# Kernel tuning notes

Hardware: AMD Instinct MI355X
Metric: run time of the kernel (lower is better)

The kernel has to match this reference:

```python
import jax, jax.numpy as jnp
import numpy as np

B, N, IN_CH = 16, 2048, 128
H, C = 4, 64
HC = H * C
E = 524288
NT = B * N
FC0, FC1 = 1024, 512
OMIC = 128
OUT = 2
LN_EPS = 1e-5


def setup_inputs() -> dict:
    key = jax.random.key(0)
    ks = jax.random.split(key, 32)
    s = 0.02
    d = {}
    d['x'] = jax.random.normal(ks[0], (NT, IN_CH), jnp.float32)
    d['edge_index'] = jax.random.randint(ks[1], (2, E), 0, NT, dtype=jnp.int64)
    # GATConv 1: Linear(IN_CH, H*C, bias=False), att_src/att_dst [H,C], bias [H*C]
    d['w1'] = jax.random.normal(ks[2], (IN_CH, HC), jnp.float32) * s
    d['att_src1'] = jax.random.normal(ks[3], (H, C), jnp.float32) * s
    d['att_dst1'] = jax.random.normal(ks[4], (H, C), jnp.float32) * s
    d['bias1'] = jnp.zeros((HC,), jnp.float32)
    d['pool1_w'] = jax.random.normal(ks[5], (HC, 1), jnp.float32) * s
    d['pool1_b'] = jnp.zeros((1,), jnp.float32)
    # GATConv 2: in = H*C
    d['w2'] = jax.random.normal(ks[6], (HC, HC), jnp.float32) * s
    d['att_src2'] = jax.random.normal(ks[7], (H, C), jnp.float32) * s
    d['att_dst2'] = jax.random.normal(ks[8], (H, C), jnp.float32) * s
    d['bias2'] = jnp.zeros((HC,), jnp.float32)
    d['pool2_w'] = jax.random.normal(ks[9], (HC, 1), jnp.float32) * s
    d['pool2_b'] = jnp.zeros((1,), jnp.float32)
    # LayerNorm(num_nodes)
    d['ln_w'] = jnp.ones((N,), jnp.float32)
    d['ln_b'] = jnp.zeros((N,), jnp.float32)
    # FC encoder: Linear(3N, FC0)+ELU, Linear(FC0, FC1)+ELU, Linear(FC1, OMIC)+ELU
    d['enc0_w'] = jax.random.normal(ks[10], (3 * N, FC0), jnp.float32) * s
    d['enc0_b'] = jnp.zeros((FC0,), jnp.float32)
    d['enc1_w'] = jax.random.normal(ks[11], (FC0, FC1), jnp.float32) * s
    d['enc1_b'] = jnp.zeros((FC1,), jnp.float32)
    d['enc2_w'] = jax.random.normal(ks[12], (FC1, OMIC), jnp.float32) * s
    d['enc2_b'] = jnp.zeros((OMIC,), jnp.float32)
    d['last_w'] = jax.random.normal(ks[13], (OMIC, OUT), jnp.float32) * s
    d['last_b'] = jnp.zeros((OUT,), jnp.float32)
    return d


def layer_norm(v, w, b):
    mu = jnp.mean(v, axis=-1, keepdims=True)
    var = jnp.mean((v - mu) ** 2, axis=-1, keepdims=True)
    return (v - mu) * jax.lax.rsqrt(var + LN_EPS) * w + b


def gat_conv(x, src, dst, w, att_src, att_dst, bias):
    # x: [NT, F_in] -> transformed per head [NT, H, C]
    xw = (x @ w).reshape(NT, H, C)
    a_src = jnp.einsum('nhc,hc->nh', xw, att_src)  # [NT, H]
    a_dst = jnp.einsum('nhc,hc->nh', xw, att_dst)
    alpha = jax.nn.leaky_relu(a_src[src] + a_dst[dst], negative_slope=0.2)  # [E', H]
    amax = jax.ops.segment_max(alpha, dst, num_segments=NT)
    ea = jnp.exp(alpha - amax[dst])
    denom = jax.ops.segment_sum(ea, dst, num_segments=NT)
    coef = ea / (denom[dst] + 1e-16)
    msg = xw[src] * coef[:, :, None]  # [E', H, C]
    out = jax.ops.segment_sum(msg, dst, num_segments=NT)
    return out.reshape(NT, HC) + bias


def reference(x, edge_index, w1, att_src1, att_dst1, bias1, pool1_w, pool1_b,
              w2, att_src2, att_dst2, bias2, pool2_w, pool2_b,
              ln_w, ln_b, enc0_w, enc0_b, enc1_w, enc1_b, enc2_w, enc2_b,
              last_w, last_b):
    # add self-loops (GATConv default)
    loops = jnp.arange(NT, dtype=edge_index.dtype)
    src = jnp.concatenate([edge_index[0], loops])
    dst = jnp.concatenate([edge_index[1], loops])
    # layer1 feature: per-node mean, densified to [B, N]
    x0 = layer_norm(jnp.mean(x, axis=-1).reshape(B, N), ln_w, ln_b)
    # GAT layer 1 (dropout is identity in eval)
    h = jax.nn.elu(gat_conv(x, src, dst, w1, att_src1, att_dst1, bias1))
    x1 = layer_norm((h @ pool1_w + pool1_b)[:, 0].reshape(B, N), ln_w, ln_b)
    # GAT layer 2
    h = jax.nn.elu(gat_conv(h, src, dst, w2, att_src2, att_dst2, bias2))
    x2 = layer_norm((h @ pool2_w + pool2_b)[:, 0].reshape(B, N), ln_w, ln_b)
    feat = jnp.concatenate([x0, x1, x2], axis=1)  # [B, 3N]
    e = jax.nn.elu(feat @ enc0_w + enc0_b)
    e = jax.nn.elu(e @ enc1_w + enc1_b)
    e = jax.nn.elu(e @ enc2_w + enc2_b)
    return e @ last_w + last_b  # [B, OUT]
```

## Files before the change

kernel.cpp:

```cpp
#include <hip/hip_runtime.h>
#include <math.h>

#define NTN 32768
#define BB 16
#define NN 2048
#define IN_CH 128
#define HC 256
#define EREAL 524288
#define ETOT (EREAL + NTN)
#define FC0 1024
#define FC1 512
#define OMIC 128
#define OUTD 2
#define CAP 96

#define PREP_BLKS (NTN / 4)
#define DEG_BLKS (EREAL / 256)
#define CASTW_BLKS ((HC * IN_CH + HC * HC) / 256)
#define GEMM_YB (NTN / 128)
#define FILL_YB 512

typedef __attribute__((ext_vector_type(8))) short bf16x8;
typedef __attribute__((ext_vector_type(4))) float f32x4;
typedef __attribute__((ext_vector_type(2))) float f32x2;

static __device__ __forceinline__ float wave_sum(float v) {
    for (int o = 32; o; o >>= 1) v += __shfl_xor(v, o);
    return v;
}
static __device__ __forceinline__ unsigned short f2bf(float f) {
    unsigned u = __float_as_uint(f);
    unsigned r = (u + 0x7fff + ((u >> 16) & 1)) >> 16;
    return (unsigned short)r;
}
static __device__ __forceinline__ void wave_sync() {
    asm volatile("s_waitcnt lgkmcnt(0)" ::: "memory");
    __builtin_amdgcn_sched_barrier(0);
}
static __device__ __forceinline__ void pkfma(f32x2& acc, f32x2 ab, f32x2 e2) {
    asm("v_pk_fma_f32 %0, %1, %2, %0" : "+v"(acc) : "v"(ab), "v"(e2));
}
static __device__ __forceinline__ void fma8pk(uint4 v, f32x2 e2, f32x2* acc) {
    f32x2 p;
    p.x = __uint_as_float(v.x << 16); p.y = __uint_as_float(v.x & 0xffff0000u);
    pkfma(acc[0], p, e2);
    p.x = __uint_as_float(v.y << 16); p.y = __uint_as_float(v.y & 0xffff0000u);
    pkfma(acc[1], p, e2);
    p.x = __uint_as_float(v.z << 16); p.y = __uint_as_float(v.z & 0xffff0000u);
    pkfma(acc[2], p, e2);
    p.x = __uint_as_float(v.w << 16); p.y = __uint_as_float(v.w & 0xffff0000u);
    pkfma(acc[3], p, e2);
}
static __device__ __forceinline__ void dot2bf(float& acc, unsigned px, unsigned pe) {
    asm("v_dot2_f32_bf16 %0, %1, %2, %0" : "+v"(acc) : "v"(px), "v"(pe));
}
static __device__ __forceinline__ void dot8x2(uint4 a, uint4 b, unsigned pe, float* acc) {
    unsigned p;
    p = __builtin_amdgcn_perm(a.x, b.x, 0x01000504u); dot2bf(acc[0], p, pe);
    p = __builtin_amdgcn_perm(a.x, b.x, 0x03020706u); dot2bf(acc[1], p, pe);
    p = __builtin_amdgcn_perm(a.y, b.y, 0x01000504u); dot2bf(acc[2], p, pe);
    p = __builtin_amdgcn_perm(a.y, b.y, 0x03020706u); dot2bf(acc[3], p, pe);
    p = __builtin_amdgcn_perm(a.z, b.z, 0x01000504u); dot2bf(acc[4], p, pe);
    p = __builtin_amdgcn_perm(a.z, b.z, 0x03020706u); dot2bf(acc[5], p, pe);
    p = __builtin_amdgcn_perm(a.w, b.w, 0x01000504u); dot2bf(acc[6], p, pe);
    p = __builtin_amdgcn_perm(a.w, b.w, 0x03020706u); dot2bf(acc[7], p, pe);
}

__global__ __launch_bounds__(256) void k_pre(
    const float* __restrict__ x, unsigned short* __restrict__ xb, float* __restrict__ xmean,
    const int* __restrict__ ei, int* __restrict__ deg, int* __restrict__ epos,
    const float* __restrict__ w1, const float* __restrict__ w2,
    unsigned short* __restrict__ w1t, unsigned short* __restrict__ w2t) {
    int b = blockIdx.x, t = threadIdx.x;
    if (b < PREP_BLKS) {
        int wave = t >> 6, lane = t & 63;
        int n = b * 4 + wave;
        float2 v = *(const float2*)(x + (size_t)n * IN_CH + lane * 2);
        ushort2 o;
        o.x = f2bf(v.x); o.y = f2bf(v.y);
        *(ushort2*)(xb + (size_t)n * IN_CH + lane * 2) = o;
        float s = wave_sum(v.x + v.y);
        if (lane == 0) xmean[n] = s * (1.0f / 128.0f);
    } else if (b < PREP_BLKS + DEG_BLKS) {
        int e = (b - PREP_BLKS) * 256 + t;
        int d = ei[EREAL + e];
        epos[e] = atomicAdd(&deg[d], 1);
    } else {
        int idx = (b - PREP_BLKS - DEG_BLKS) * 256 + t;
        if (idx < HC * IN_CH) {
            int n = idx / IN_CH, k = idx % IN_CH;
            w1t[idx] = f2bf(w1[(size_t)k * HC + n]);
        } else {
            int j = idx - HC * IN_CH;
            int n = j / HC, k = j % HC;
            w2t[j] = f2bf(w2[(size_t)k * HC + n]);
        }
    }
}

__global__ __launch_bounds__(1024) void k_scan(const int* __restrict__ deg, int* __restrict__ rowptr,
                                               int* __restrict__ csr) {
    __shared__ int sd[1024];
    int t = threadIdx.x;
    int base = t * 32;
    int loc[32];
    int s = 0;
#pragma unroll
    for (int j = 0; j < 32; j++) { int d = deg[base + j] + 1; loc[j] = d; s += d; }
    sd[t] = s; __syncthreads();
    for (int o = 1; o < 1024; o <<= 1) {
        int v = (t >= o) ? sd[t - o] : 0;
        __syncthreads();
        sd[t] += v;
        __syncthreads();
    }
    int run = sd[t] - s;
#pragma unroll
    for (int j = 0; j < 32; j++) {
        rowptr[base + j] = run;
        csr[run] = base + j;
        run += loc[j];
    }
    if (t == 1023) rowptr[NTN] = run;
}

__global__ __launch_bounds__(256) void k_gemm_mfma(
    const unsigned short* __restrict__ A, const unsigned short* __restrict__ Bt, int K,
    const float* __restrict__ attS, const float* __restrict__ attD,
    unsigned short* __restrict__ Cout, float* __restrict__ aS, float* __restrict__ aD,
    const int* __restrict__ ei, const int* __restrict__ epos,
    const int* __restrict__ rowptr, int* __restrict__ csr) {
    __shared__ unsigned short As[128][72];
    __shared__ unsigned short Bs[64][72];
    const int t = threadIdx.x;
    const int bx = blockIdx.x, by = blockIdx.y;
    if (by >= GEMM_YB) {
        int e = (((by - GEMM_YB) * 4 + bx)) * 256 + t;
        int s = ei[e], d = ei[EREAL + e];
        csr[rowptr[d] + 1 + epos[e]] = s;
        return;
    }
    const int lane = t & 63, wave = t >> 6;
    const int quad = lane >> 4, l16 = lane & 15;
    const int arow = t >> 1, acol = (t & 1) * 32;
    const int brow = t >> 2, bcol = (t & 3) * 16;
    const unsigned short* Ag = A + (size_t)(by * 128 + arow) * K + acol;
    const unsigned short* Bg = Bt + (size_t)(bx * 64 + brow) * K + bcol;
    f32x4 acc[2][4] = {};
    for (int k0 = 0; k0 < K; k0 += 64) {
        uint4 a0 = *(const uint4*)(Ag + k0);
        uint4 a1 = *(const uint4*)(Ag + k0 + 8);
        uint4 a2 = *(const uint4*)(Ag + k0 + 16);
        uint4 a3 = *(const uint4*)(Ag + k0 + 24);
        uint4 b0 = *(const uint4*)(Bg + k0);
        uint4 b1 = *(const uint4*)(Bg + k0 + 8);
        __syncthreads();
        *(uint4*)&As[arow][acol +  0] = a0;
        *(uint4*)&As[arow][acol +  8] = a1;
        *(uint4*)&As[arow][acol + 16] = a2;
        *(uint4*)&As[arow][acol + 24] = a3;
        *(uint4*)&Bs[brow][bcol +  0] = b0;
        *(uint4*)&Bs[brow][bcol +  8] = b1;
        __syncthreads();
#pragma unroll
        for (int kc = 0; kc < 64; kc += 32) {
            bf16x8 af[2], bfr[4];
#pragma unroll
            for (int mt = 0; mt < 2; mt++)
                af[mt] = *(const bf16x8*)&As[wave * 32 + mt * 16 + l16][kc + quad * 8];
#pragma unroll
            for (int nt = 0; nt < 4; nt++)
                bfr[nt] = *(const bf16x8*)&Bs[nt * 16 + l16][kc + quad * 8];
#pragma unroll
            for (int mt = 0; mt < 2; mt++)
#pragma unroll
                for (int nt = 0; nt < 4; nt++)
                    acc[mt][nt] = __builtin_amdgcn_mfma_f32_16x16x32_bf16(af[mt], bfr[nt], acc[mt][nt], 0, 0, 0);
        }
    }
    float as_l[4], ad_l[4];
#pragma unroll
    for (int nt = 0; nt < 4; nt++) {
        int gcol = bx * 64 + nt * 16 + l16;
        as_l[nt] = attS[gcol];
        ad_l[nt] = attD[gcol];
    }
#pragma unroll
    for (int mt = 0; mt < 2; mt++) {
#pragma unroll
        for (int reg = 0; reg < 4; reg++) {
            int grow = by * 128 + wave * 32 + mt * 16 + quad * 4 + reg;
            float ps = 0.f, pd = 0.f;
#pragma unroll
            for (int nt = 0; nt < 4; nt++) {
                float v = acc[mt][nt][reg];
                Cout[(size_t)grow * HC + bx * 64 + nt * 16 + l16] = f2bf(v);
                ps += v * as_l[nt];
                pd += v * ad_l[nt];
            }
            for (int o = 8; o; o >>= 1) { ps += __shfl_xor(ps, o); pd += __shfl_xor(pd, o); }
            if (l16 == 0) { aS[grow * 4 + bx] = ps; aD[grow * 4 + bx] = pd; }
        }
    }
}

__global__ __launch_bounds__(256) void k_agg(
    const unsigned short* __restrict__ xw, const float* __restrict__ aS, const float* __restrict__ aD,
    const int* __restrict__ rowptr, const int* __restrict__ csr,
    const float* __restrict__ bias, const float* __restrict__ poolw, const float* __restrict__ poolb,
    unsigned short* __restrict__ hout, float* __restrict__ xpre) {
    __shared__ float ea_s[4][CAP][4];
    __shared__ int   ss[4][CAP];
    int t = threadIdx.x;
    int w = t >> 6, lane = t & 63;
    int n = blockIdx.x * 4 + w;
    int beg = rowptr[n], end = rowptr[n + 1];
    int deg = end - beg;
    float4 ad4 = *(const float4*)(aD + n * 4);
    float l0 = 0.f, l1 = 0.f, l2 = 0.f, l3 = 0.f;
    if (deg <= CAP) {
        for (int i = lane; i < deg; i += 64) {
            int s = csr[beg + i];
            ss[w][i] = s << 9;
            float4 as4 = *(const float4*)(aS + s * 4);
            float a0 = as4.x + ad4.x; a0 = a0 > 0.f ? a0 : 0.2f * a0;
            float a1 = as4.y + ad4.y; a1 = a1 > 0.f ? a1 : 0.2f * a1;
            float a2 = as4.z + ad4.z; a2 = a2 > 0.f ? a2 : 0.2f * a2;
            float a3 = as4.w + ad4.w; a3 = a3 > 0.f ? a3 : 0.2f * a3;
            float4 e4;
            e4.x = __expf(a0); e4.y = __expf(a1); e4.z = __expf(a2); e4.w = __expf(a3);
            *(float4*)&ea_s[w][i][0] = e4;
        }
        wave_sync();
    } else {
        for (int i = lane; i < deg; i += 64) {
            int s = csr[beg + i];
            float4 as4 = *(const float4*)(aS + s * 4);
            float a0 = as4.x + ad4.x; a0 = a0 > 0.f ? a0 : 0.2f * a0; l0 += __expf(a0);
            float a1 = as4.y + ad4.y; a1 = a1 > 0.f ? a1 : 0.2f * a1; l1 += __expf(a1);
            float a2 = as4.z + ad4.z; a2 = a2 > 0.f ? a2 : 0.2f * a2; l2 += __expf(a2);
            float a3 = as4.w + ad4.w; a3 = a3 > 0.f ? a3 : 0.2f * a3; l3 += __expf(a3);
        }
        l0 = wave_sum(l0); l1 = wave_sum(l1); l2 = wave_sum(l2); l3 = wave_sum(l3);
    }
    int l31 = lane & 31, hi = lane >> 5;
    int head = l31 >> 3;
    float acc8[8] = {};
    f32x2 accF[4] = {};
    unsigned tb = (unsigned)(l31 * 16);
    const char* xwb_ = (const char*)xw;
    if (deg <= CAP) {
        int i = 0;
        for (; i + 16 <= deg; i += 16) {
            int iA = i + 8 * hi;
            int o0 = ss[w][iA], o1 = ss[w][iA + 1], o2 = ss[w][iA + 2], o3 = ss[w][iA + 3];
            int o4 = ss[w][iA + 4], o5 = ss[w][iA + 5], o6 = ss[w][iA + 6], o7 = ss[w][iA + 7];
            float e0 = ea_s[w][iA][head],     e1 = ea_s[w][iA + 1][head];
            float e2 = ea_s[w][iA + 2][head], e3 = ea_s[w][iA + 3][head];
            float e4 = ea_s[w][iA + 4][head], e5 = ea_s[w][iA + 5][head];
            float e6 = ea_s[w][iA + 6][head], e7 = ea_s[w][iA + 7][head];
            uint4 v0 = *(const uint4*)(xwb_ + ((unsigned)o0 + tb));
            uint4 v1 = *(const uint4*)(xwb_ + ((unsigned)o1 + tb));
            uint4 v2 = *(const uint4*)(xwb_ + ((unsigned)o2 + tb));
            uint4 v3 = *(const uint4*)(xwb_ + ((unsigned)o3 + tb));
            uint4 v4 = *(const uint4*)(xwb_ + ((unsigned)o4 + tb));
            uint4 v5 = *(const uint4*)(xwb_ + ((unsigned)o5 + tb));
            uint4 v6 = *(const uint4*)(xwb_ + ((unsigned)o6 + tb));
            uint4 v7 = *(const uint4*)(xwb_ + ((unsigned)o7 + tb));
            unsigned p01, p23, p45, p67;
            asm("v_cvt_pk_bf16_f32 %0, %1, %2" : "=v"(p01) : "v"(e0), "v"(e1));
            asm("v_cvt_pk_bf16_f32 %0, %1, %2" : "=v"(p23) : "v"(e2), "v"(e3));
            asm("v_cvt_pk_bf16_f32 %0, %1, %2" : "=v"(p45) : "v"(e4), "v"(e5));
            asm("v_cvt_pk_bf16_f32 %0, %1, %2" : "=v"(p67) : "v"(e6), "v"(e7));
            dot8x2(v0, v1, p01, acc8);
            dot8x2(v2, v3, p23, acc8);
            dot8x2(v4, v5, p45, acc8);
            dot8x2(v6, v7, p67, acc8);
        }
        for (; i + 8 <= deg; i += 8) {
            int iA = i + 4 * hi;
            int o0 = ss[w][iA], o1 = ss[w][iA + 1], o2 = ss[w][iA + 2], o3 = ss[w][iA + 3];
            float e0 = ea_s[w][iA][head],     e1 = ea_s[w][iA + 1][head];
            float e2 = ea_s[w][iA + 2][head], e3 = ea_s[w][iA + 3][head];
            uint4 v0 = *(const uint4*)(xwb_ + ((unsigned)o0 + tb));
            uint4 v1 = *(const uint4*)(xwb_ + ((unsigned)o1 + tb));
            uint4 v2 = *(const uint4*)(xwb_ + ((unsigned)o2 + tb));
            uint4 v3 = *(const uint4*)(xwb_ + ((unsigned)o3 + tb));
            unsigned p01, p23;
            asm("v_cvt_pk_bf16_f32 %0, %1, %2" : "=v"(p01) : "v"(e0), "v"(e1));
            asm("v_cvt_pk_bf16_f32 %0, %1, %2" : "=v"(p23) : "v"(e2), "v"(e3));
            dot8x2(v0, v1, p01, acc8);
            dot8x2(v2, v3, p23, acc8);
        }
        for (; i + 4 <= deg; i += 4) {
            int iA = i + 2 * hi;
            int o0 = ss[w][iA], o1 = ss[w][iA + 1];
            float e0 = ea_s[w][iA][head], e1 = ea_s[w][iA + 1][head];
            unsigned pe;
            asm("v_cvt_pk_bf16_f32 %0, %1, %2" : "=v"(pe) : "v"(e0), "v"(e1));
            uint4 v0 = *(const uint4*)(xwb_ + ((unsigned)o0 + tb));
            uint4 v1 = *(const uint4*)(xwb_ + ((unsigned)o1 + tb));
            dot8x2(v0, v1, pe, acc8);
        }
        if (i < deg) {
            int iA = i + 2 * hi, iB = iA + 1;
            bool okA = iA < deg, okB = iB < deg;
            int ia = okA ? iA : 0;
            int ib = okB ? iB : 0;
            int o0 = ss[w][ia], o1 = ss[w][ib];
            float e0 = okA ? ea_s[w][ia][head] : 0.f;
            float e1 = okB ? ea_s[w][ib][head] : 0.f;
            unsigned pe;
            asm("v_cvt_pk_bf16_f32 %0, %1, %2" : "=v"(pe) : "v"(e0), "v"(e1));
            uint4 v0 = *(const uint4*)(xwb_ + ((unsigned)o0 + tb));
            uint4 v1 = *(const uint4*)(xwb_ + ((unsigned)o1 + tb));
            dot8x2(v0, v1, pe, acc8);
        }
    } else {
        const unsigned short* xwc = xw + l31 * 8;
        float adh = head == 0 ? ad4.x : head == 1 ? ad4.y : head == 2 ? ad4.z : ad4.w;
        for (int i = beg; i < end; i += 2) {
            int idx = i + hi;
            bool ok = idx < end;
            int sA = csr[ok ? idx : beg];
            float a = aS[sA * 4 + head] + adh;
            a = a > 0.f ? a : 0.2f * a;
            float eA = ok ? __expf(a) : 0.f;
            uint4 vA = *(const uint4*)(xwc + (size_t)sA * HC);
            f32x2 eA2; eA2.x = eA; eA2.y = eA;
            fma8pk(vA, eA2, accF);
        }
    }
    float r8[8];
#pragma unroll
    for (int j = 0; j < 8; j++) {
        float v = acc8[j] + accF[j >> 1][j & 1];
        v += __shfl_xor(v, 32);
        r8[j] = v;
    }
    if (hi == 0) {
        float ilh;
        if (deg <= CAP) {
            float lsum = 0.f;
            for (int j = (l31 & 7); j < deg; j += 8) lsum += ea_s[w][j][head];
            lsum += __shfl_xor(lsum, 1);
            lsum += __shfl_xor(lsum, 2);
            lsum += __shfl_xor(lsum, 4);
            ilh = 1.0f / (lsum + 1e-16f);
        } else {
            float lh = head == 0 ? l0 : head == 1 ? l1 : head == 2 ? l2 : l3;
            ilh = 1.0f / (lh + 1e-16f);
        }
        float4 b0 = *(const float4*)(bias + l31 * 8);
        float4 b1 = *(const float4*)(bias + l31 * 8 + 4);
        float r[8];
        r[0] = r8[0] * ilh + b0.x;
        r[1] = r8[1] * ilh + b0.y;
        r[2] = r8[2] * ilh + b0.z;
        r[3] = r8[3] * ilh + b0.w;
        r[4] = r8[4] * ilh + b1.x;
        r[5] = r8[5] * ilh + b1.y;
        r[6] = r8[6] * ilh + b1.z;
        r[7] = r8[7] * ilh + b1.w;
#pragma unroll
        for (int j = 0; j < 8; j++) r[j] = r[j] > 0.f ? r[j] : expm1f(r[j]);
        if (hout) {
            uint4 o;
            o.x = (unsigned)f2bf(r[0]) | ((unsigned)f2bf(r[1]) << 16);
            o.y = (unsigned)f2bf(r[2]) | ((unsigned)f2bf(r[3]) << 16);
            o.z = (unsigned)f2bf(r[4]) | ((unsigned)f2bf(r[5]) << 16);
            o.w = (unsigned)f2bf(r[6]) | ((unsigned)f2bf(r[7]) << 16);
            *(uint4*)(hout + (size_t)n * HC + l31 * 8) = o;
        }
        float4 w0 = *(const float4*)(poolw + l31 * 8);
        float4 w1v = *(const float4*)(poolw + l31 * 8 + 4);
        float p = r[0] * w0.x + r[1] * w0.y + r[2] * w0.z + r[3] * w0.w +
                  r[4] * w1v.x + r[5] * w1v.y + r[6] * w1v.z + r[7] * w1v.w;
        for (int o = 16; o; o >>= 1) p += __shfl_xor(p, o);
        if (l31 == 0) xpre[n] = p + poolb[0];
    }
}

__global__ __launch_bounds__(256) void k_ln3(const float* __restrict__ xmean, const float* __restrict__ x1pre,
                                             const float* __restrict__ x2pre, const float* __restrict__ lw,
                                             const float* __restrict__ lb, float* __restrict__ feat) {
    __shared__ float r0[256], r1[256];
    int b = blockIdx.x, t = threadIdx.x;
    int row = b & 15, seg = b >> 4;
    const float* src = (seg == 0 ? xmean : seg == 1 ? x1pre : x2pre) + (size_t)row * NN;
    float* dst = feat + (size_t)row * (3 * NN) + seg * NN;
    float v[8];
    float s = 0.f, s2 = 0.f;
#pragma unroll
    for (int j = 0; j < 8; j++) {
        float x = src[t + j * 256];
        v[j] = x; s += x; s2 += x * x;
    }
    r0[t] = s; r1[t] = s2; __syncthreads();
    for (int o = 128; o; o >>= 1) {
        if (t < o) { r0[t] += r0[t + o]; r1[t] += r1[t + o]; }
        __syncthreads();
    }
    float mu = r0[0] * (1.0f / NN);
    float var = r1[0] * (1.0f / NN) - mu * mu;
    float rs = rsqrtf(var + 1e-5f);
#pragma unroll
    for (int j = 0; j < 8; j++) {
        int idx = t + j * 256;
        dst[idx] = (v[j] - mu) * rs * lw[idx] + lb[idx];
    }
}

template<int KC>
__global__ __launch_bounds__(256) void k_fc_splitk(const float* __restrict__ In, const float* __restrict__ W,
                                                   float* __restrict__ partial, int K, int Nc) {
    __shared__ float in_s[16][KC];
    int t = threadIdx.x;
    int k0 = blockIdx.y * KC;
    for (int idx = t; idx < 16 * KC; idx += 256) {
        int r = idx / KC, kk = idx % KC;
        in_s[r][kk] = In[(size_t)r * K + k0 + kk];
    }
    __syncthreads();
    int col = blockIdx.x * 256 + t;
    if (col < Nc) {
        float acc[16] = {};
#pragma unroll
        for (int kk = 0; kk < KC; kk++) {
            float w = W[(size_t)(k0 + kk) * Nc + col];
#pragma unroll
            for (int r = 0; r < 16; r++) acc[r] += in_s[r][kk] * w;
        }
        float* pp = partial + ((size_t)blockIdx.y * 16) * Nc + col;
#pragma unroll
        for (int r = 0; r < 16; r++) pp[(size_t)r * Nc] = acc[r];
    }
}

__global__ __launch_bounds__(256) void k_fc1(
    const float* __restrict__ part0, const float* __restrict__ b0,
    const float* __restrict__ W, float* __restrict__ partial) {
    __shared__ float in_s[16][16];
    int t = threadIdx.x;
    int bx = blockIdx.x, by = blockIdx.y;
    int k0 = by * 16;
    {
        int r = t >> 4, kk = t & 15;
        float s = 0.f;
#pragma unroll 8
        for (int k = 0; k < 96; k++) s += part0[((size_t)(k * 16) + r) * FC0 + (k0 + kk)];
        s += b0[k0 + kk];
        in_s[r][kk] = s > 0.f ? s : expm1f(s);
    }
    __syncthreads();
    int col = bx * 256 + t;
    float acc[16] = {};
#pragma unroll
    for (int kk = 0; kk < 16; kk++) {
        float wv = W[(size_t)(k0 + kk) * FC1 + col];
#pragma unroll
        for (int r = 0; r < 16; r++) acc[r] += in_s[r][kk] * wv;
    }
    float* pp = partial + ((size_t)by * 16) * FC1 + col;
#pragma unroll
    for (int r = 0; r < 16; r++) pp[(size_t)r * FC1] = acc[r];
}

__global__ __launch_bounds__(256) void k_fc2(
    const float* __restrict__ part1, const float* __restrict__ b1,
    const float* __restrict__ W, float* __restrict__ partial) {
    __shared__ float in_s[16][16];
    int t = threadIdx.x;
    int by = blockIdx.x;
    int k0 = by * 16;
    {
        int r = t >> 4, kk = t & 15;
        float s = 0.f;
#pragma unroll 8
        for (int k = 0; k < 64; k++) s += part1[((size_t)(k * 16) + r) * FC1 + (k0 + kk)];
        s += b1[k0 + kk];
        in_s[r][kk] = s > 0.f ? s : expm1f(s);
    }
    __syncthreads();
    if (t < OMIC) {
        int col = t;
        float acc[16] = {};
#pragma unroll
        for (int kk = 0; kk < 16; kk++) {
            float wv = W[(size_t)(k0 + kk) * OMIC + col];
#pragma unroll
            for (int r = 0; r < 16; r++) acc[r] += in_s[r][kk] * wv;
        }
        float* pp = partial + ((size_t)by * 16) * OMIC + col;
#pragma unroll
        for (int r = 0; r < 16; r++) pp[(size_t)r * OMIC] = acc[r];
    }
}

__global__ __launch_bounds__(256) void k_last2(
    const float* __restrict__ part2, const float* __restrict__ b2,
    const float* __restrict__ W, const float* __restrict__ bl, float* __restrict__ Out) {
    __shared__ float e2s[16][OMIC];
    int t = threadIdx.x;
    for (int idx = t; idx < 16 * OMIC; idx += 256) {
        int r = idx >> 7, c = idx & 127;
        float s = 0.f;
#pragma unroll 8
        for (int k = 0; k < 32; k++) s += part2[((size_t)(k * 16) + r) * OMIC + c];
        s += b2[c];
        e2s[r][c] = s > 0.f ? s : expm1f(s);
    }
    __syncthreads();
    int r = t >> 4, c = (t >> 3) & 1, ksub = t & 7;
    float s = 0.f;
#pragma unroll
    for (int k = 0; k < OMIC / 8; k++) s += e2s[r][k * 8 + ksub] * W[(k * 8 + ksub) * OUTD + c];
    for (int o = 1; o < 8; o <<= 1) s += __shfl_xor(s, o);
    if (ksub == 0) Out[r * OUTD + c] = s + bl[c];
}

extern "C" void kernel_launch(void* const* d_in, const int* in_sizes, int n_in,
                              void* d_out, int out_size, void* d_ws, size_t ws_size,
                              hipStream_t stream) {
    (void)in_sizes; (void)n_in; (void)out_size; (void)ws_size;
    const float* x        = (const float*)d_in[0];
    const int*   ei       = (const int*)d_in[1];
    const float* w1       = (const float*)d_in[2];
    const float* att_src1 = (const float*)d_in[3];
    const float* att_dst1 = (const float*)d_in[4];
    const float* bias1    = (const float*)d_in[5];
    const float* pool1_w  = (const float*)d_in[6];
    const float* pool1_b  = (const float*)d_in[7];
    const float* w2       = (const float*)d_in[8];
    const float* att_src2 = (const float*)d_in[9];
    const float* att_dst2 = (const float*)d_in[10];
    const float* bias2    = (const float*)d_in[11];
    const float* pool2_w  = (const float*)d_in[12];
    const float* pool2_b  = (const float*)d_in[13];
    const float* ln_w     = (const float*)d_in[14];
    const float* ln_b     = (const float*)d_in[15];
    const float* enc0_w   = (const float*)d_in[16];
    const float* enc0_b   = (const float*)d_in[17];
    const float* enc1_w   = (const float*)d_in[18];
    const float* enc1_b   = (const float*)d_in[19];
    const float* enc2_w   = (const float*)d_in[20];
    const float* enc2_b   = (const float*)d_in[21];
    const float* last_w   = (const float*)d_in[22];
    const float* last_b   = (const float*)d_in[23];
    float* out = (float*)d_out;

    char* p = (char*)d_ws;
    auto alloc = [&](size_t bytes) -> void* {
        void* r = (void*)p;
        p += (bytes + 255) & ~(size_t)255;
        return r;
    };
    unsigned short* xwb  = (unsigned short*)alloc((size_t)NTN * HC * 2);
    unsigned short* hb   = (unsigned short*)alloc((size_t)NTN * HC * 2);
    unsigned short* xb   = (unsigned short*)alloc((size_t)NTN * IN_CH * 2);
    unsigned short* w1t  = (unsigned short*)alloc((size_t)HC * IN_CH * 2);
    unsigned short* w2t  = (unsigned short*)alloc((size_t)HC * HC * 2);
    float* a_src  = (float*)alloc((size_t)NTN * 4 * 4);
    float* a_dst  = (float*)alloc((size_t)NTN * 4 * 4);
    float* xmean  = (float*)alloc((size_t)NTN * 4);
    float* x1pre  = (float*)alloc((size_t)NTN * 4);
    float* x2pre  = (float*)alloc((size_t)NTN * 4);
    float* feat   = (float*)alloc((size_t)BB * 3 * NN * 4);
    float* part0  = (float*)alloc((size_t)96 * 16 * FC0 * 4);
    float* part1  = (float*)alloc((size_t)64 * 16 * FC1 * 4);
    float* part2  = (float*)alloc((size_t)32 * 16 * OMIC * 4);
    int*   deg    = (int*)alloc((size_t)NTN * 4);
    int*   rowptr = (int*)alloc((size_t)(NTN + 1) * 4);
    int*   epos   = (int*)alloc((size_t)EREAL * 4);
    int*   csr    = (int*)alloc((size_t)ETOT * 4);

    hipMemsetAsync(deg, 0, (size_t)NTN * 4, stream);

    k_pre<<<PREP_BLKS + DEG_BLKS + CASTW_BLKS, 256, 0, stream>>>(
        x, xb, xmean, ei, deg, epos, w1, w2, w1t, w2t);
    k_scan<<<1, 1024, 0, stream>>>(deg, rowptr, csr);

    k_gemm_mfma<<<dim3(4, GEMM_YB + FILL_YB), 256, 0, stream>>>(
        xb, w1t, IN_CH, att_src1, att_dst1, xwb, a_src, a_dst, ei, epos, rowptr, csr);
    k_agg<<<NTN / 4, 256, 0, stream>>>(xwb, a_src, a_dst, rowptr, csr, bias1, pool1_w, pool1_b, hb, x1pre);

    k_gemm_mfma<<<dim3(4, GEMM_YB), 256, 0, stream>>>(
        hb, w2t, HC, att_src2, att_dst2, xwb, a_src, a_dst, ei, epos, rowptr, csr);
    k_agg<<<NTN / 4, 256, 0, stream>>>(xwb, a_src, a_dst, rowptr, csr, bias2, pool2_w, pool2_b, (unsigned short*)nullptr, x2pre);

    k_ln3<<<48, 256, 0, stream>>>(xmean, x1pre, x2pre, ln_w, ln_b, feat);
    k_fc_splitk<64><<<dim3(4, 96), 256, 0, stream>>>(feat, enc0_w, part0, 3 * NN, FC0);
    k_fc1<<<dim3(2, 64), 256, 0, stream>>>(part0, enc0_b, enc1_w, part1);
    k_fc2<<<32, 256, 0, stream>>>(part1, enc1_b, enc2_w, part2);
    k_last2<<<1, 256, 0, stream>>>(part2, enc2_b, last_w, last_b, out);
}
```

Baseline: 330.4 us.

## Widen GEMM tile to full 256 columns and pack bf16 output stores

The projection GEMM now has each block compute a 128x256 tile covering all heads, instead of a 4-wide grid of 64-column tiles. Each A tile is loaded once rather than four times, and the attention logits for all four heads are written as one float4 per row. Output bf16 values are paired through a lane shuffle so each store writes 32 bits. In exchange, accumulator registers grow to 32 f32x4 per thread and LDS rises to about 55KB, which may lower occupancy, and there are four times fewer GEMM blocks.

```diff
diff --git a/kernel.cpp b/kernel.cpp
--- a/kernel.cpp
+++ b/kernel.cpp
@@ -17,8 +17,8 @@
 #define PREP_BLKS (NTN / 4)
 #define DEG_BLKS (EREAL / 256)
 #define CASTW_BLKS ((HC * IN_CH + HC * HC) / 256)
-#define GEMM_YB (NTN / 128)
-#define FILL_YB 512
+#define GEMM_BLKS (NTN / 128)
+#define FILL_BLKS (EREAL / 256)
 
 typedef __attribute__((ext_vector_type(8))) short bf16x8;
 typedef __attribute__((ext_vector_type(4))) float f32x4;
@@ -131,11 +131,11 @@
     const int* __restrict__ ei, const int* __restrict__ epos,
     const int* __restrict__ rowptr, int* __restrict__ csr) {
     __shared__ unsigned short As[128][72];
-    __shared__ unsigned short Bs[64][72];
+    __shared__ unsigned short Bs[256][72];
     const int t = threadIdx.x;
-    const int bx = blockIdx.x, by = blockIdx.y;
-    if (by >= GEMM_YB) {
-        int e = (((by - GEMM_YB) * 4 + bx)) * 256 + t;
+    const int bid = blockIdx.x;
+    if (bid >= GEMM_BLKS) {
+        int e = (bid - GEMM_BLKS) * 256 + t;
         int s = ei[e], d = ei[EREAL + e];
         csr[rowptr[d] + 1 + epos[e]] = s;
         return;
@@ -143,10 +143,9 @@
     const int lane = t & 63, wave = t >> 6;
     const int quad = lane >> 4, l16 = lane & 15;
     const int arow = t >> 1, acol = (t & 1) * 32;
-    const int brow = t >> 2, bcol = (t & 3) * 16;
-    const unsigned short* Ag = A + (size_t)(by * 128 + arow) * K + acol;
-    const unsigned short* Bg = Bt + (size_t)(bx * 64 + brow) * K + bcol;
-    f32x4 acc[2][4] = {};
+    const unsigned short* Ag = A + (size_t)(bid * 128 + arow) * K + acol;
+    const unsigned short* Bg = Bt + (size_t)t * K;
+    f32x4 acc[2][16] = {};
     for (int k0 = 0; k0 < K; k0 += 64) {
         uint4 a0 = *(const uint4*)(Ag + k0);
         uint4 a1 = *(const uint4*)(Ag + k0 + 8);
@@ -154,34 +153,42 @@
         uint4 a3 = *(const uint4*)(Ag + k0 + 24);
         uint4 b0 = *(const uint4*)(Bg + k0);
         uint4 b1 = *(const uint4*)(Bg + k0 + 8);
+        uint4 b2 = *(const uint4*)(Bg + k0 + 16);
+        uint4 b3 = *(const uint4*)(Bg + k0 + 24);
+        uint4 b4 = *(const uint4*)(Bg + k0 + 32);
+        uint4 b5 = *(const uint4*)(Bg + k0 + 40);
+        uint4 b6 = *(const uint4*)(Bg + k0 + 48);
+        uint4 b7 = *(const uint4*)(Bg + k0 + 56);
         __syncthreads();
         *(uint4*)&As[arow][acol +  0] = a0;
         *(uint4*)&As[arow][acol +  8] = a1;
         *(uint4*)&As[arow][acol + 16] = a2;
         *(uint4*)&As[arow][acol + 24] = a3;
-        *(uint4*)&Bs[brow][bcol +  0] = b0;
-        *(uint4*)&Bs[brow][bcol +  8] = b1;
+        *(uint4*)&Bs[t][ 0] = b0;
+        *(uint4*)&Bs[t][ 8] = b1;
+        *(uint4*)&Bs[t][16] = b2;
+        *(uint4*)&Bs[t][24] = b3;
+        *(uint4*)&Bs[t][32] = b4;
+        *(uint4*)&Bs[t][40] = b5;
+        *(uint4*)&Bs[t][48] = b6;
+        *(uint4*)&Bs[t][56] = b7;
         __syncthreads();
 #pragma unroll
         for (int kc = 0; kc < 64; kc += 32) {
-            bf16x8 af[2], bfr[4];
-#pragma unroll
-            for (int mt = 0; mt < 2; mt++)
-                af[mt] = *(const bf16x8*)&As[wave * 32 + mt * 16 + l16][kc + quad * 8];
-#pragma unroll
-            for (int nt = 0; nt < 4; nt++)
-                bfr[nt] = *(const bf16x8*)&Bs[nt * 16 + l16][kc + quad * 8];
-#pragma unroll
-            for (int mt = 0; mt < 2; mt++)
-#pragma unroll
-                for (int nt = 0; nt < 4; nt++)
-                    acc[mt][nt] = __builtin_amdgcn_mfma_f32_16x16x32_bf16(af[mt], bfr[nt], acc[mt][nt], 0, 0, 0);
-        }
-    }
-    float as_l[4], ad_l[4];
-#pragma unroll
-    for (int nt = 0; nt < 4; nt++) {
-        int gcol = bx * 64 + nt * 16 + l16;
+            bf16x8 af0 = *(const bf16x8*)&As[wave * 32 + l16][kc + quad * 8];
+            bf16x8 af1 = *(const bf16x8*)&As[wave * 32 + 16 + l16][kc + quad * 8];
+#pragma unroll
+            for (int nt = 0; nt < 16; nt++) {
+                bf16x8 bfr = *(const bf16x8*)&Bs[nt * 16 + l16][kc + quad * 8];
+                acc[0][nt] = __builtin_amdgcn_mfma_f32_16x16x32_bf16(af0, bfr, acc[0][nt], 0, 0, 0);
+                acc[1][nt] = __builtin_amdgcn_mfma_f32_16x16x32_bf16(af1, bfr, acc[1][nt], 0, 0, 0);
+            }
+        }
+    }
+    float as_l[16], ad_l[16];
+#pragma unroll
+    for (int nt = 0; nt < 16; nt++) {
+        int gcol = nt * 16 + l16;
         as_l[nt] = attS[gcol];
         ad_l[nt] = attD[gcol];
     }
@@ -189,17 +196,32 @@
     for (int mt = 0; mt < 2; mt++) {
 #pragma unroll
         for (int reg = 0; reg < 4; reg++) {
-            int grow = by * 128 + wave * 32 + mt * 16 + quad * 4 + reg;
-            float ps = 0.f, pd = 0.f;
-#pragma unroll
-            for (int nt = 0; nt < 4; nt++) {
+            int grow = bid * 128 + wave * 32 + mt * 16 + quad * 4 + reg;
+            float ph[4] = {0.f, 0.f, 0.f, 0.f}, pd[4] = {0.f, 0.f, 0.f, 0.f};
+#pragma unroll
+            for (int nt = 0; nt < 16; nt++) {
                 float v = acc[mt][nt][reg];
-                Cout[(size_t)grow * HC + bx * 64 + nt * 16 + l16] = f2bf(v);
-                ps += v * as_l[nt];
-                pd += v * ad_l[nt];
+                unsigned u = (unsigned)f2bf(v);
+                unsigned un = __shfl_xor(u, 1);
+                if (!(l16 & 1))
+                    *(unsigned*)(Cout + (size_t)grow * HC + nt * 16 + l16) = u | (un << 16);
+                int h = nt >> 2;
+                ph[h] += v * as_l[nt];
+                pd[h] += v * ad_l[nt];
             }
-            for (int o = 8; o; o >>= 1) { ps += __shfl_xor(ps, o); pd += __shfl_xor(pd, o); }
-            if (l16 == 0) { aS[grow * 4 + bx] = ps; aD[grow * 4 + bx] = pd; }
+#pragma unroll
+            for (int h = 0; h < 4; h++) {
+                for (int o = 8; o; o >>= 1) {
+                    ph[h] += __shfl_xor(ph[h], o);
+                    pd[h] += __shfl_xor(pd[h], o);
+                }
+            }
+            if (l16 == 0) {
+                float4 sv; sv.x = ph[0]; sv.y = ph[1]; sv.z = ph[2]; sv.w = ph[3];
+                float4 dv; dv.x = pd[0]; dv.y = pd[1]; dv.z = pd[2]; dv.w = pd[3];
+                *(float4*)(aS + (size_t)grow * 4) = sv;
+                *(float4*)(aD + (size_t)grow * 4) = dv;
+            }
         }
     }
 }
@@ -580,11 +602,11 @@
         x, xb, xmean, ei, deg, epos, w1, w2, w1t, w2t);
     k_scan<<<1, 1024, 0, stream>>>(deg, rowptr, csr);
 
-    k_gemm_mfma<<<dim3(4, GEMM_YB + FILL_YB), 256, 0, stream>>>(
+    k_gemm_mfma<<<GEMM_BLKS + FILL_BLKS, 256, 0, stream>>>(
         xb, w1t, IN_CH, att_src1, att_dst1, xwb, a_src, a_dst, ei, epos, rowptr, csr);
     k_agg<<<NTN / 4, 256, 0, stream>>>(xwb, a_src, a_dst, rowptr, csr, bias1, pool1_w, pool1_b, hb, x1pre);
 
-    k_gemm_mfma<<<dim3(4, GEMM_YB), 256, 0, stream>>>(
+    k_gemm_mfma<<<GEMM_BLKS, 256, 0, stream>>>(
         hb, w2t, HC, att_src2, att_dst2, xwb, a_src, a_dst, ei, epos, rowptr, csr);
     k_agg<<<NTN / 4, 256, 0, stream>>>(xwb, a_src, a_dst, rowptr, csr, bias2, pool2_w, pool2_b, (unsigned short*)nullptr, x2pre);
 
```

New measurement: 348.7 us. 1.06x slower.
